# Performance work log

Measured on AMD Instinct MI355X. Metric: run time of the kernel, lower is better.

The kernel has to match this reference:

```python
import math
import jax, jax.numpy as jnp
import numpy as np

D = 512        # encoder_dim
LLM = 4096     # llm_dim
H = 8          # heads
L = 2          # depth
FF = 4 * D     # feedforward hidden
DH = D // H    # head dim
EPS = 1e-5


def setup_inputs() -> dict:
    key = jax.random.key(0)
    ks = jax.random.split(key, 16)
    s_d = 1.0 / math.sqrt(D)
    s_ff = 1.0 / math.sqrt(FF)
    inp = {
        "x": jax.random.normal(ks[0], (1, 8192, D), dtype=jnp.float32),
        # per-layer params, leading dim L
        "ln1_g": jnp.ones((L, D), jnp.float32),
        "ln1_b": jnp.zeros((L, D), jnp.float32),
        "Wq": jax.random.normal(ks[1], (L, D, D), jnp.float32) * s_d,
        "Wk": jax.random.normal(ks[2], (L, D, D), jnp.float32) * s_d,
        "Wv": jax.random.normal(ks[3], (L, D, D), jnp.float32) * s_d,
        "Wo": jax.random.normal(ks[4], (L, D, D), jnp.float32) * s_d,
        "bo": jnp.zeros((L, D), jnp.float32),
        "ln2_g": jnp.ones((L, D), jnp.float32),
        "ln2_b": jnp.zeros((L, D), jnp.float32),
        "W1": jax.random.normal(ks[5], (L, D, FF), jnp.float32) * s_d,
        "b1": jnp.zeros((L, FF), jnp.float32),
        "W2": jax.random.normal(ks[6], (L, FF, D), jnp.float32) * s_ff,
        "b2": jnp.zeros((L, D), jnp.float32),
        # final projector (xavier-like)
        "proj_W": jax.random.normal(ks[7], (D, LLM), jnp.float32) * math.sqrt(2.0 / (D + LLM)),
        "proj_b": jnp.zeros((LLM,), jnp.float32),
    }
    return inp


def _layernorm(h, g, b):
    mu = jnp.mean(h, axis=-1, keepdims=True)
    var = jnp.var(h, axis=-1, keepdims=True)
    return (h - mu) * jax.lax.rsqrt(var + EPS) * g + b


def _sinusoidal_pe(n, d):
    pos = jnp.arange(n, dtype=jnp.float32)[:, None]
    div = jnp.exp(jnp.arange(0, d, 2, dtype=jnp.float32) * (-math.log(10000.0) / d))
    pe = jnp.zeros((n, d), jnp.float32)
    pe = pe.at[:, 0::2].set(jnp.sin(pos * div))
    pe = pe.at[:, 1::2].set(jnp.cos(pos * div))
    return pe


def reference(x, ln1_g, ln1_b, Wq, Wk, Wv, Wo, bo, ln2_g, ln2_b, W1, b1, W2, b2, proj_W, proj_b):
    B, N, _ = x.shape
    x = x + _sinusoidal_pe(N, D)[None]  # positional encoding (dropout = identity at eval)
    scale = DH ** -0.5
    for l in range(L):
        # --- linear self-attention block (PreNorm + residual) ---
        h = _layernorm(x, ln1_g[l], ln1_b[l])
        q = (h @ Wq[l]).reshape(B, N, H, DH).transpose(0, 2, 1, 3)  # bhnd
        k = (h @ Wk[l]).reshape(B, N, H, DH).transpose(0, 2, 1, 3)
        v = (h @ Wv[l]).reshape(B, N, H, DH).transpose(0, 2, 1, 3)
        q = jax.nn.softmax(q, axis=-1) * scale        # softmax over feature dim
        k = jax.nn.softmax(k, axis=-2)                # softmax over sequence dim
        ctx = jnp.einsum('bhnd,bhne->bhde', k, v)     # small [B,H,DH,DH] context
        o = jnp.einsum('bhnd,bhde->bhne', q, ctx)
        o = o.transpose(0, 2, 1, 3).reshape(B, N, D)
        x = x + (o @ Wo[l] + bo[l])
        # --- feedforward block (PreNorm + residual, exact GELU) ---
        h = _layernorm(x, ln2_g[l], ln2_b[l])
        x = x + (jax.nn.gelu(h @ W1[l] + b1[l], approximate=False) @ W2[l] + b2[l])
    x = jnp.squeeze(x, 0)  # batch==1, matches torch x.squeeze(0)
    return x @ proj_W + proj_b  # [N, LLM]
```

## Files before the change

### kernel.cpp

```cpp
#include <hip/hip_runtime.h>
#include <hip/hip_bf16.h>
#include <math.h>

constexpr int N_SEQ = 8192;
constexpr int D     = 512;
constexpr int NH    = 8;
constexpr int FFDIM = 2048;
constexpr int LLMD  = 4096;
constexpr int NLAYER= 2;

typedef __bf16 bf16x8 __attribute__((ext_vector_type(8)));
typedef float  f32x4  __attribute__((ext_vector_type(4)));
typedef unsigned short u16x8 __attribute__((ext_vector_type(8)));

__device__ __forceinline__ unsigned short f2bf(float x) {
  unsigned u = __builtin_bit_cast(unsigned, x);
  unsigned r = (u + 0x7FFFu + ((u >> 16) & 1u)) >> 16;
  return (unsigned short)r;
}
__device__ __forceinline__ float bf2f(unsigned short u) {
  unsigned x = ((unsigned)u) << 16;
  return __builtin_bit_cast(float, x);
}

#define GLOAD16(g, l)                                                        \
  __builtin_amdgcn_global_load_lds(                                          \
      (const __attribute__((address_space(1))) void*)(g),                    \
      (__attribute__((address_space(3))) void*)(l), 16, 0, 0)

__global__ __launch_bounds__(256) void prep_kernel(const float* __restrict__ Wq,
                                                   const float* __restrict__ Wk,
                                                   const float* __restrict__ Wv,
                                                   const float* __restrict__ Wo,
                                                   const float* __restrict__ W1,
                                                   const float* __restrict__ W2,
                                                   const float* __restrict__ Wp,
                                                   unsigned short* __restrict__ WT,
                                                   const float* __restrict__ xin,
                                                   unsigned short* __restrict__ Xr,
                                                   unsigned short* __restrict__ Hb,
                                                   const float* __restrict__ g,
                                                   const float* __restrict__ b) {
  int bid = blockIdx.x;
  if (bid >= 8192) {
    int row  = ((bid - 8192) * 256 + (int)threadIdx.x) >> 6;
    int lane = threadIdx.x & 63;
    const float* p = xin + (size_t)row * D + lane * 8;
    float x[8];
#pragma unroll
    for (int i = 0; i < 8; ++i) {
      int d = lane * 8 + i;
      float freq = __expf((float)(d & ~1) * (-9.210340371976184f / 512.0f));
      float arg = (float)row * freq;
      float pe = (d & 1) ? cosf(arg) : sinf(arg);
      x[i] = p[i] + pe;
    }
    float s = 0.f, sq = 0.f;
#pragma unroll
    for (int i = 0; i < 8; ++i) { s += x[i]; sq += x[i] * x[i]; }
#pragma unroll
    for (int o = 32; o > 0; o >>= 1) { s += __shfl_xor(s, o); sq += __shfl_xor(sq, o); }
    float mu  = s * (1.0f / D);
    float var = sq * (1.0f / D) - mu * mu;
    float rs  = rsqrtf(var + 1e-5f);
    u16x8 xr, r;
#pragma unroll
    for (int i = 0; i < 8; ++i) {
      xr[i] = f2bf(x[i]);
      r[i]  = f2bf((x[i] - mu) * rs * g[lane * 8 + i] + b[lane * 8 + i]);
    }
    *(u16x8*)(Xr + (size_t)row * D + lane * 8) = xr;
    *(u16x8*)(Hb + (size_t)row * D + lane * 8) = r;
    return;
  }
  const float* src; unsigned short* dst; int K, N, tile;
  if (bid < 2048) {
    int mat = bid >> 8; int w = mat >> 1, l = mat & 1;
    const float* s4 = (w == 0) ? Wq : (w == 1) ? Wk : (w == 2) ? Wv : Wo;
    src = s4 + (size_t)l * 262144;
    dst = WT + ((size_t)l * 4 + w) * 262144;
    K = 512; N = 512; tile = bid & 255;
  } else if (bid < 4096) {
    int b2 = bid - 2048; int l = b2 >> 10;
    src = W1 + (size_t)l * 1048576; dst = WT + 2097152 + (size_t)l * 1048576;
    K = 512; N = 2048; tile = b2 & 1023;
  } else if (bid < 6144) {
    int b2 = bid - 4096; int l = b2 >> 10;
    src = W2 + (size_t)l * 1048576; dst = WT + 4194304 + (size_t)l * 1048576;
    K = 2048; N = 512; tile = b2 & 1023;
  } else {
    src = Wp; dst = WT + 6291456; K = 512; N = 4096; tile = bid - 6144;
  }
  int tilesN = N >> 5;
  int bk = (tile / tilesN) << 5, bn = (tile % tilesN) << 5;
  __shared__ float s[32][33];
  int r = threadIdx.x >> 5, c = threadIdx.x & 31;
#pragma unroll
  for (int i = 0; i < 4; ++i)
    s[r + 8 * i][c] = src[(size_t)(bk + r + 8 * i) * N + bn + c];
  __syncthreads();
#pragma unroll
  for (int i = 0; i < 4; ++i) {
    int rr = r + 8 * i;
    dst[(size_t)(bn + rr) * K + bk + c] = f2bf(s[c][rr]);
  }
}

__global__ __launch_bounds__(256) void ln_bf16(const unsigned short* __restrict__ in,
                                               unsigned short* __restrict__ out,
                                               const float* __restrict__ g,
                                               const float* __restrict__ b) {
  int row  = (blockIdx.x * 256 + threadIdx.x) >> 6;
  int lane = threadIdx.x & 63;
  u16x8 v = *(const u16x8*)(in + (size_t)row * D + lane * 8);
  float x[8];
#pragma unroll
  for (int i = 0; i < 8; ++i) x[i] = bf2f(v[i]);
  float s = 0.f, sq = 0.f;
#pragma unroll
  for (int i = 0; i < 8; ++i) { s += x[i]; sq += x[i] * x[i]; }
#pragma unroll
  for (int o = 32; o > 0; o >>= 1) { s += __shfl_xor(s, o); sq += __shfl_xor(sq, o); }
  float mu  = s * (1.0f / D);
  float var = sq * (1.0f / D) - mu * mu;
  float rs  = rsqrtf(var + 1e-5f);
  f32x4 g0 = *(const f32x4*)(g + lane * 8);
  f32x4 g1 = *(const f32x4*)(g + lane * 8 + 4);
  f32x4 b0 = *(const f32x4*)(b + lane * 8);
  f32x4 b1 = *(const f32x4*)(b + lane * 8 + 4);
  u16x8 r;
#pragma unroll
  for (int i = 0; i < 4; ++i) r[i]     = f2bf((x[i] - mu) * rs * g0[i] + b0[i]);
#pragma unroll
  for (int i = 0; i < 4; ++i) r[i + 4] = f2bf((x[i + 4] - mu) * rs * g1[i] + b1[i]);
  *(u16x8*)(out + (size_t)row * D + lane * 8) = r;
}

template <int FLAGS, int BN>
__global__ __launch_bounds__(256) void mgemm2(const unsigned short* __restrict__ A,
                                              const unsigned short* __restrict__ Bt,
                                              const float* __restrict__ bias,
                                              const unsigned short* __restrict__ resb,
                                              float* __restrict__ C,
                                              unsigned short* __restrict__ Cb,
                                              int M, int N, int K) {
  constexpr int WNI  = BN / 32;
  constexpr int NBUF = (BN == 128) ? 3 : 4;
  __shared__ unsigned short As[NBUF][128][32];
  __shared__ unsigned short Bs[NBUF][BN][32];
  const int tid = threadIdx.x;
  const int lane = tid & 63, wv = tid >> 6;
  const int nwg = gridDim.x * gridDim.y;
  int bid = blockIdx.y * gridDim.x + blockIdx.x;
  bid = (bid & 7) * (nwg >> 3) + (bid >> 3);
  const int bm = (bid / gridDim.x) * 128, bn = (bid % gridDim.x) * BN;
  const int wr = (wv >> 1) * 64, wc = (wv & 1) * (BN / 2);
  f32x4 acc[4][WNI] = {};

  const int srA = wv * 32 + (lane >> 2);
  const int sc  = (lane & 3) * 8;
  const unsigned short* Ap0 = A + (size_t)(bm + srA) * K + sc;
  const unsigned short* Ap1 = Ap0 + (size_t)16 * K;
  const int srB = wv * (BN / 4) + (lane >> 2);
  const unsigned short* Bp0 = Bt + (size_t)(bn + srB) * K + sc;
  const unsigned short* Bp1 = Bp0 + (size_t)16 * K;
  const int kh = (lane >> 4) * 8;
  const int fr = lane & 15;

  auto stage = [&](int bb, int k0) {
    GLOAD16(Ap0 + k0, &As[bb][srA][sc]);
    GLOAD16(Ap1 + k0, &As[bb][srA + 16][sc]);
    GLOAD16(Bp0 + k0, &Bs[bb][srB][sc]);
    if constexpr (BN == 128) GLOAD16(Bp1 + k0, &Bs[bb][srB + 16][sc]);
  };

  const int nt = K >> 5;
#pragma unroll
  for (int i = 0; i < NBUF - 1; ++i) stage(i, i << 5);
  int cur = 0;
  for (int t = 0; t < nt; ++t) {
    __builtin_amdgcn_sched_barrier(0);
    if constexpr (BN == 128)
      asm volatile("s_waitcnt vmcnt(4)" ::: "memory");
    else
      asm volatile("s_waitcnt vmcnt(6)" ::: "memory");
    __builtin_amdgcn_s_barrier();
    __builtin_amdgcn_sched_barrier(0);
    bf16x8 af[4], bfv[WNI];
#pragma unroll
    for (int mi = 0; mi < 4; ++mi)
      af[mi] = *(const bf16x8*)&As[cur][wr + mi * 16 + fr][kh];
#pragma unroll
    for (int ni = 0; ni < WNI; ++ni)
      bfv[ni] = *(const bf16x8*)&Bs[cur][wc + ni * 16 + fr][kh];
    if (t + NBUF - 1 < nt) {
      int tgt = cur - 1; if (tgt < 0) tgt += NBUF;
      stage(tgt, (t + NBUF - 1) << 5);
    }
#pragma unroll
    for (int mi = 0; mi < 4; ++mi)
#pragma unroll
      for (int ni = 0; ni < WNI; ++ni)
        acc[mi][ni] = __builtin_amdgcn_mfma_f32_16x16x32_bf16(af[mi], bfv[ni], acc[mi][ni], 0, 0, 0);
    ++cur; if (cur == NBUF) cur = 0;
  }

  const int r4 = (lane >> 4) * 4, cc = lane & 15;
#pragma unroll
  for (int mi = 0; mi < 4; ++mi) {
#pragma unroll
    for (int ni = 0; ni < WNI; ++ni) {
      int col = bn + wc + ni * 16 + cc;
      float bsv = (FLAGS & 1) ? bias[col] : 0.0f;
      f32x4 v = acc[mi][ni];
#pragma unroll
      for (int j = 0; j < 4; ++j) {
        int row = bm + wr + mi * 16 + r4 + j;
        float x = v[j] + bsv;
        if (FLAGS & 2) x = 0.5f * x * (1.0f + erff(x * 0.7071067811865475f));
        if (FLAGS & 4) x += bf2f(resb[(size_t)row * N + col]);
        if (!(FLAGS & 16)) C[(size_t)row * N + col] = x;
        if (FLAGS & 8) Cb[(size_t)row * N + col] = f2bf(x);
      }
    }
  }
}

__global__ __launch_bounds__(256) void qkv_gemm(const unsigned short* __restrict__ A,
                                                const unsigned short* __restrict__ Bt,
                                                unsigned short* __restrict__ Qb,
                                                unsigned short* __restrict__ Kb,
                                                unsigned short* __restrict__ Vb,
                                                float* __restrict__ pm,
                                                float* __restrict__ ps) {
  constexpr int K = 512;
  __shared__ unsigned short As[3][128][32];
  __shared__ unsigned short Bs[3][128][32];
  const int tid = threadIdx.x;
  const int lane = tid & 63, wv = tid >> 6;
  const int nwg = gridDim.x * gridDim.y;
  int bid = blockIdx.y * gridDim.x + blockIdx.x;
  bid = (bid & 7) * (nwg >> 3) + (bid >> 3);
  const int bm = (bid / gridDim.x) * 128, bn = (bid % gridDim.x) * 128;
  const int bmy = bid / gridDim.x;
  const int wr = (wv >> 1) * 64, wc = (wv & 1) * 64;
  f32x4 acc[4][4] = {};

  const int srA = wv * 32 + (lane >> 2);
  const int sc  = (lane & 3) * 8;
  const unsigned short* Ap0 = A + (size_t)(bm + srA) * K + sc;
  const unsigned short* Ap1 = Ap0 + (size_t)16 * K;
  const unsigned short* Bp0 = Bt + (size_t)(bn + srA) * K + sc;
  const unsigned short* Bp1 = Bp0 + (size_t)16 * K;
  const int kh = (lane >> 4) * 8;
  const int fr = lane & 15;

  auto stage = [&](int bb, int k0) {
    GLOAD16(Ap0 + k0, &As[bb][srA][sc]);
    GLOAD16(Ap1 + k0, &As[bb][srA + 16][sc]);
    GLOAD16(Bp0 + k0, &Bs[bb][srA][sc]);
    GLOAD16(Bp1 + k0, &Bs[bb][srA + 16][sc]);
  };

  stage(0, 0);
  stage(1, 32);
  int cur = 0;
  for (int t = 0; t < 16; ++t) {
    __builtin_amdgcn_sched_barrier(0);
    asm volatile("s_waitcnt vmcnt(4)" ::: "memory");
    __builtin_amdgcn_s_barrier();
    __builtin_amdgcn_sched_barrier(0);
    bf16x8 af[4], bfv[4];
#pragma unroll
    for (int mi = 0; mi < 4; ++mi)
      af[mi] = *(const bf16x8*)&As[cur][wr + mi * 16 + fr][kh];
#pragma unroll
    for (int ni = 0; ni < 4; ++ni)
      bfv[ni] = *(const bf16x8*)&Bs[cur][wc + ni * 16 + fr][kh];
    if (t + 2 < 16) {
      int tgt = cur - 1; if (tgt < 0) tgt += 3;
      stage(tgt, (t + 2) << 5);
    }
#pragma unroll
    for (int mi = 0; mi < 4; ++mi)
#pragma unroll
      for (int ni = 0; ni < 4; ++ni)
        acc[mi][ni] = __builtin_amdgcn_mfma_f32_16x16x32_bf16(af[mi], bfv[ni], acc[mi][ni], 0, 0, 0);
    ++cur; if (cur == 3) cur = 0;
  }

  const int r4 = (lane >> 4) * 4, cc = lane & 15;
  if (bn < 512) {
#pragma unroll
    for (int mi = 0; mi < 4; ++mi) {
#pragma unroll
      for (int j = 0; j < 4; ++j) {
        float v0 = acc[mi][0][j], v1 = acc[mi][1][j];
        float v2 = acc[mi][2][j], v3 = acc[mi][3][j];
        float m = fmaxf(fmaxf(v0, v1), fmaxf(v2, v3));
        m = fmaxf(m, __shfl_xor(m, 1)); m = fmaxf(m, __shfl_xor(m, 2));
        m = fmaxf(m, __shfl_xor(m, 4)); m = fmaxf(m, __shfl_xor(m, 8));
        float e0 = __expf(v0 - m), e1 = __expf(v1 - m);
        float e2 = __expf(v2 - m), e3 = __expf(v3 - m);
        float s = e0 + e1 + e2 + e3;
        s += __shfl_xor(s, 1); s += __shfl_xor(s, 2);
        s += __shfl_xor(s, 4); s += __shfl_xor(s, 8);
        float w = 0.125f / s;
        int row = bm + wr + mi * 16 + r4 + j;
        unsigned short* qr = Qb + (size_t)row * 512 + bn + wc + cc;
        qr[0] = f2bf(e0 * w); qr[16] = f2bf(e1 * w);
        qr[32] = f2bf(e2 * w); qr[48] = f2bf(e3 * w);
      }
    }
  } else if (bn < 1024) {
    int colb = bn - 512 + wc + cc;
    int prow = bmy * 2 + (wr ? 1 : 0);
#pragma unroll
    for (int ni = 0; ni < 4; ++ni) {
      float kf[4][4];
      float m = -1e30f;
#pragma unroll
      for (int mi = 0; mi < 4; ++mi)
#pragma unroll
        for (int j = 0; j < 4; ++j) {
          unsigned short kr = f2bf(acc[mi][ni][j]);
          Kb[(size_t)(bm + wr + mi * 16 + r4 + j) * 512 + colb + ni * 16] = kr;
          kf[mi][j] = bf2f(kr);
          m = fmaxf(m, kf[mi][j]);
        }
      m = fmaxf(m, __shfl_xor(m, 16));
      m = fmaxf(m, __shfl_xor(m, 32));
      float s = 0.f;
#pragma unroll
      for (int mi = 0; mi < 4; ++mi)
#pragma unroll
        for (int j = 0; j < 4; ++j) s += __expf(kf[mi][j] - m);
      s += __shfl_xor(s, 16);
      s += __shfl_xor(s, 32);
      if (lane < 16) {
        pm[(size_t)prow * 512 + colb + ni * 16] = m;
        ps[(size_t)prow * 512 + colb + ni * 16] = s;
      }
    }
  } else {
    int colv = bn - 1024 + wc + cc;
#pragma unroll
    for (int mi = 0; mi < 4; ++mi)
#pragma unroll
      for (int ni = 0; ni < 4; ++ni) {
        f32x4 v = acc[mi][ni];
#pragma unroll
        for (int j = 0; j < 4; ++j)
          Vb[(size_t)(bm + wr + mi * 16 + r4 + j) * 512 + colv + ni * 16] = f2bf(v[j]);
      }
  }
}

__global__ __launch_bounds__(256) void ctx_kernel(const unsigned short* __restrict__ kb,
                                                  const unsigned short* __restrict__ vb,
                                                  const float* __restrict__ pm,
                                                  const float* __restrict__ ps,
                                                  float* __restrict__ part) {
  int chunk = blockIdx.x, h = blockIdx.y, t = threadIdx.x;
  __shared__ unsigned short kst[64 * 256];
  __shared__ unsigned short vst[64 * 256];
  __shared__ float qm[4][64], qsum[4][64], scm[64], sci[64];
  {
    int c = t & 63, qt = t >> 6;
    float m = -1e30f, s = 0.f;
    for (int r = qt * 32; r < qt * 32 + 32; ++r) {
      float vm = pm[(size_t)r * 512 + h * 64 + c];
      float vp = ps[(size_t)r * 512 + h * 64 + c];
      float nm = fmaxf(m, vm);
      s = s * __expf(m - nm) + vp * __expf(vm - nm);
      m = nm;
    }
    qm[qt][c] = m; qsum[qt][c] = s;
  }
  __syncthreads();
  if (t < 64) {
    float M = fmaxf(fmaxf(qm[0][t], qm[1][t]), fmaxf(qm[2][t], qm[3][t]));
    float S = qsum[0][t] * __expf(qm[0][t] - M) + qsum[1][t] * __expf(qm[1][t] - M)
            + qsum[2][t] * __expf(qm[2][t] - M) + qsum[3][t] * __expf(qm[3][t] - M);
    scm[t] = M; sci[t] = 1.0f / S;
  }
  __syncthreads();
  size_t rowbase = (size_t)chunk * 256;
  for (int i = t; i < 4096; i += 256) {
    int n = i >> 4, c4 = (i & 15) * 4;
    ushort4 k4 = *(const ushort4*)&kb[(rowbase + n) * 512 + h * 64 + c4];
    ushort4 v4 = *(const ushort4*)&vb[(rowbase + n) * 512 + h * 64 + c4];
    unsigned short kr[4] = {
      f2bf(__expf(bf2f(k4.x) - scm[c4 + 0]) * sci[c4 + 0]),
      f2bf(__expf(bf2f(k4.y) - scm[c4 + 1]) * sci[c4 + 1]),
      f2bf(__expf(bf2f(k4.z) - scm[c4 + 2]) * sci[c4 + 2]),
      f2bf(__expf(bf2f(k4.w) - scm[c4 + 3]) * sci[c4 + 3])};
    unsigned short vr[4] = {v4.x, v4.y, v4.z, v4.w};
#pragma unroll
    for (int j = 0; j < 4; ++j) {
      int d = c4 + j;
      int byt = (d * 512 + n * 2) ^ ((d & 7) << 4);
      *(unsigned short*)((char*)kst + byt) = kr[j];
      *(unsigned short*)((char*)vst + byt) = vr[j];
    }
  }
  __syncthreads();
  int lane = t & 63, wv = t >> 6;
  int fr = lane & 15, kh = (lane >> 4) * 8;
  f32x4 acc[4] = {};
  int d = wv * 16 + fr;
#pragma unroll
  for (int kk = 0; kk < 8; ++kk) {
    int abyt = (d * 512 + (kk * 32 + kh) * 2) ^ ((d & 7) << 4);
    bf16x8 af = *(const bf16x8*)((const char*)kst + abyt);
#pragma unroll
    for (int ni = 0; ni < 4; ++ni) {
      int e = ni * 16 + fr;
      int bbyt = (e * 512 + (kk * 32 + kh) * 2) ^ ((e & 7) << 4);
      bf16x8 bv = *(const bf16x8*)((const char*)vst + bbyt);
      acc[ni] = __builtin_amdgcn_mfma_f32_16x16x32_bf16(af, bv, acc[ni], 0, 0, 0);
    }
  }
  int r4 = (lane >> 4) * 4, cc = lane & 15;
  float* pb = &part[((size_t)h * 32 + chunk) * 4096];
#pragma unroll
  for (int ni = 0; ni < 4; ++ni)
#pragma unroll
    for (int j = 0; j < 4; ++j)
      pb[(wv * 16 + r4 + j) * 64 + ni * 16 + cc] = acc[ni][j];
}

__global__ __launch_bounds__(256) void ctx_reduce_kernel(const float* __restrict__ part,
                                                         float* __restrict__ ctx) {
  int idx = blockIdx.x * 256 + threadIdx.x;
  int h = idx >> 12, de = idx & 4095;
  float s = 0.f;
#pragma unroll 8
  for (int c = 0; c < 32; ++c) s += part[((size_t)h * 32 + c) * 4096 + de];
  ctx[(size_t)h * 4096 + de] = s;
}

__global__ __launch_bounds__(256) void ctxw2_kernel(const float* __restrict__ ctx,
                                                    const float* __restrict__ Wo,
                                                    unsigned short* __restrict__ WPT) {
  int ct = blockIdx.x, h = blockIdx.y, t = threadIdx.x;
  __shared__ float cs[64][64];
  __shared__ float wo[64][64];
  for (int i = t; i < 4096; i += 256) {
    cs[i >> 6][i & 63] = ctx[(size_t)h * 4096 + i];
    wo[i >> 6][i & 63] = Wo[(size_t)(h * 64 + (i >> 6)) * 512 + ct * 64 + (i & 63)];
  }
  __syncthreads();
  int cl = t & 63, dg = (t >> 6) * 16;
  float accv[16];
#pragma unroll
  for (int j = 0; j < 16; ++j) accv[j] = 0.f;
  for (int e = 0; e < 64; ++e) {
    float w = wo[e][cl];
#pragma unroll
    for (int j = 0; j < 16; ++j) accv[j] = fmaf(cs[dg + j][e], w, accv[j]);
  }
  u16x8 o0, o1;
#pragma unroll
  for (int j = 0; j < 8; ++j) { o0[j] = f2bf(accv[j]); o1[j] = f2bf(accv[j + 8]); }
  unsigned short* dst = WPT + (size_t)(ct * 64 + cl) * 512 + h * 64 + dg;
  *(u16x8*)dst = o0;
  *(u16x8*)(dst + 8) = o1;
}

extern "C" void kernel_launch(void* const* d_in, const int* in_sizes, int n_in,
                              void* d_out, int out_size, void* d_ws, size_t ws_size,
                              hipStream_t stream) {
  const float* x_in  = (const float*)d_in[0];
  const float* ln1_g = (const float*)d_in[1];
  const float* ln1_b = (const float*)d_in[2];
  const float* Wq    = (const float*)d_in[3];
  const float* Wk    = (const float*)d_in[4];
  const float* Wv    = (const float*)d_in[5];
  const float* Wo    = (const float*)d_in[6];
  const float* bo    = (const float*)d_in[7];
  const float* ln2_g = (const float*)d_in[8];
  const float* ln2_b = (const float*)d_in[9];
  const float* W1    = (const float*)d_in[10];
  const float* b1    = (const float*)d_in[11];
  const float* W2    = (const float*)d_in[12];
  const float* b2    = (const float*)d_in[13];
  const float* projW = (const float*)d_in[14];
  const float* projb = (const float*)d_in[15];
  float* out = (float*)d_out;
  float* ws  = (float*)d_ws;
  constexpr size_t M1 = 1u << 20;

  float* CTXP = ws;
  float* PM   = ws + 1 * M1;
  float* PS   = PM + 65536;
  float* CTX  = PS + 65536;
  unsigned short* Xr  = (unsigned short*)(ws + 2 * M1);
  unsigned short* Qb  = (unsigned short*)(ws + 4 * M1);
  unsigned short* Kb  = (unsigned short*)(ws + 6 * M1);
  unsigned short* Vb  = (unsigned short*)(ws + 8 * M1);
  unsigned short* Hb  = (unsigned short*)(ws + 10 * M1);
  unsigned short* FFH = (unsigned short*)(ws + 12 * M1);
  unsigned short* WT  = (unsigned short*)(ws + 20 * M1);
  unsigned short* WPT = (unsigned short*)(ws + 24 * M1);

  prep_kernel<<<10240, 256, 0, stream>>>(Wq, Wk, Wv, Wo, W1, W2, projW, WT,
                                         x_in, Xr, Hb, ln1_g, ln1_b);

  dim3 gqkv(1536 / 128, N_SEQ / 128);
  dim3 g512n(512 / 64, N_SEQ / 128);
  dim3 gff1(FFDIM / 128, N_SEQ / 128);
  dim3 gproj(LLMD / 128, N_SEQ / 128);

  for (int l = 0; l < NLAYER; ++l) {
    const unsigned short* WQKV = WT + (size_t)l * 1048576;
    const unsigned short* W1T  = WT + 2097152 + (size_t)l * 1048576;
    const unsigned short* W2T  = WT + 4194304 + (size_t)l * 1048576;

    qkv_gemm<<<gqkv, 256, 0, stream>>>(Hb, WQKV, Qb, Kb, Vb, PM, PS);
    ctx_kernel<<<dim3(32, NH), 256, 0, stream>>>(Kb, Vb, PM, PS, CTXP);
    ctx_reduce_kernel<<<128, 256, 0, stream>>>(CTXP, CTX);
    ctxw2_kernel<<<dim3(8, NH), 256, 0, stream>>>(CTX, Wo + (size_t)l * D * D, WPT);
    mgemm2<29, 64><<<g512n, 256, 0, stream>>>(Qb, WPT, bo + l * D, Xr, nullptr,
                                              Xr, N_SEQ, 512, 512);
    ln_bf16<<<N_SEQ / 4, 256, 0, stream>>>(Xr, Hb, ln2_g + l * D, ln2_b + l * D);
    mgemm2<27, 128><<<gff1, 256, 0, stream>>>(Hb, W1T, b1 + l * FFDIM, nullptr,
                                              nullptr, FFH, N_SEQ, FFDIM, 512);
    mgemm2<29, 64><<<g512n, 256, 0, stream>>>(FFH, W2T, b2 + l * D, Xr, nullptr,
                                              Xr, N_SEQ, 512, 2048);
    if (l != NLAYER - 1)
      ln_bf16<<<N_SEQ / 4, 256, 0, stream>>>(Xr, Hb, ln1_g + (l + 1) * D,
                                             ln1_b + (l + 1) * D);
  }
  mgemm2<1, 128><<<gproj, 256, 0, stream>>>(Xr, WT + 6291456, projb, nullptr,
                                            out, nullptr, N_SEQ, LLMD, 512);
}
```

Baseline: 365.6 us.

## Fold LayerNorm into following GEMMs via row stats and gamma-scaled weights

Replaces the LayerNorm kernels that wrote a normalized bf16 activation buffer with a small row-statistics kernel that stores only mean and rstd per row. Gamma is folded into the transposed bf16 weights, and per-column sums of gamma*W and beta*W are precomputed, so the QKV and FF1 GEMMs read the raw residual and apply rs*(acc - mu*s1) + bw in the epilogue. This removes a full activation write and read per LayerNorm. The cost is an extra precompute kernel and some numerical risk, since the un-normalized residual is fed to the bf16 MMA and the mean is subtracted after accumulation (cancellation).

```diff
diff --git a/kernel.cpp b/kernel.cpp
--- a/kernel.cpp
+++ b/kernel.cpp
@@ -27,6 +27,8 @@
   __builtin_amdgcn_global_load_lds(                                          \
       (const __attribute__((address_space(1))) void*)(g),                    \
       (__attribute__((address_space(3))) void*)(l), 16, 0, 0)
+
+constexpr int SV_S1Q = 0, SV_BWQ = 3072, SV_S1F = 6144, SV_BWF = 10240;
 
 __global__ __launch_bounds__(256) void prep_kernel(const float* __restrict__ Wq,
                                                    const float* __restrict__ Wk,
@@ -38,9 +40,9 @@
                                                    unsigned short* __restrict__ WT,
                                                    const float* __restrict__ xin,
                                                    unsigned short* __restrict__ Xr,
-                                                   unsigned short* __restrict__ Hb,
-                                                   const float* __restrict__ g,
-                                                   const float* __restrict__ b) {
+                                                   float2* __restrict__ RST,
+                                                   const float* __restrict__ ln1g,
+                                                   const float* __restrict__ ln2g) {
   int bid = blockIdx.x;
   if (bid >= 8192) {
     int row  = ((bid - 8192) * 256 + (int)threadIdx.x) >> 6;
@@ -63,27 +65,27 @@
     float mu  = s * (1.0f / D);
     float var = sq * (1.0f / D) - mu * mu;
     float rs  = rsqrtf(var + 1e-5f);
-    u16x8 xr, r;
-#pragma unroll
-    for (int i = 0; i < 8; ++i) {
-      xr[i] = f2bf(x[i]);
-      r[i]  = f2bf((x[i] - mu) * rs * g[lane * 8 + i] + b[lane * 8 + i]);
-    }
+    u16x8 xr;
+#pragma unroll
+    for (int i = 0; i < 8; ++i) xr[i] = f2bf(x[i]);
     *(u16x8*)(Xr + (size_t)row * D + lane * 8) = xr;
-    *(u16x8*)(Hb + (size_t)row * D + lane * 8) = r;
+    if (lane == 0) RST[row] = make_float2(mu, rs);
     return;
   }
   const float* src; unsigned short* dst; int K, N, tile;
+  const float* gv = nullptr;
   if (bid < 2048) {
     int mat = bid >> 8; int w = mat >> 1, l = mat & 1;
     const float* s4 = (w == 0) ? Wq : (w == 1) ? Wk : (w == 2) ? Wv : Wo;
     src = s4 + (size_t)l * 262144;
     dst = WT + ((size_t)l * 4 + w) * 262144;
     K = 512; N = 512; tile = bid & 255;
+    if (w < 3) gv = ln1g + l * 512;
   } else if (bid < 4096) {
     int b2 = bid - 2048; int l = b2 >> 10;
     src = W1 + (size_t)l * 1048576; dst = WT + 2097152 + (size_t)l * 1048576;
     K = 512; N = 2048; tile = b2 & 1023;
+    gv = ln2g + l * 512;
   } else if (bid < 6144) {
     int b2 = bid - 4096; int l = b2 >> 10;
     src = W2 + (size_t)l * 1048576; dst = WT + 4194304 + (size_t)l * 1048576;
@@ -99,41 +101,64 @@
   for (int i = 0; i < 4; ++i)
     s[r + 8 * i][c] = src[(size_t)(bk + r + 8 * i) * N + bn + c];
   __syncthreads();
+  float gk = gv ? gv[bk + c] : 1.0f;
 #pragma unroll
   for (int i = 0; i < 4; ++i) {
     int rr = r + 8 * i;
-    dst[(size_t)(bn + rr) * K + bk + c] = f2bf(s[c][rr]);
-  }
-}
-
-__global__ __launch_bounds__(256) void ln_bf16(const unsigned short* __restrict__ in,
-                                               unsigned short* __restrict__ out,
-                                               const float* __restrict__ g,
-                                               const float* __restrict__ b) {
+    dst[(size_t)(bn + rr) * K + bk + c] = f2bf(s[c][rr] * gk);
+  }
+}
+
+__global__ __launch_bounds__(256) void vecprep_kernel(const float* __restrict__ Wq,
+                                                      const float* __restrict__ Wk,
+                                                      const float* __restrict__ Wv,
+                                                      const float* __restrict__ W1,
+                                                      const float* __restrict__ ln1g,
+                                                      const float* __restrict__ ln1b,
+                                                      const float* __restrict__ ln2g,
+                                                      const float* __restrict__ ln2b,
+                                                      float* __restrict__ SV) {
+  int bid = blockIdx.x, t = threadIdx.x;
+  const float* W; const float* g; const float* b;
+  int N, c0; float* s1o; float* bwo;
+  if (bid < 12) {
+    int l = bid / 6, m = (bid % 6) >> 1, chunk = bid & 1;
+    W = ((m == 0) ? Wq : (m == 1) ? Wk : Wv) + (size_t)l * 262144;
+    g = ln1g + l * 512; b = ln1b + l * 512;
+    N = 512; c0 = chunk * 256;
+    s1o = SV + SV_S1Q + l * 1536 + m * 512 + c0;
+    bwo = SV + SV_BWQ + l * 1536 + m * 512 + c0;
+  } else {
+    int b2 = bid - 12; int l = b2 >> 3, chunk = b2 & 7;
+    W = W1 + (size_t)l * 1048576;
+    g = ln2g + l * 512; b = ln2b + l * 512;
+    N = 2048; c0 = chunk * 256;
+    s1o = SV + SV_S1F + l * 2048 + c0;
+    bwo = SV + SV_BWF + l * 2048 + c0;
+  }
+  float s1 = 0.f, bw = 0.f;
+  for (int k = 0; k < 512; ++k) {
+    float w = W[(size_t)k * N + c0 + t];
+    s1 = fmaf(g[k], w, s1);
+    bw = fmaf(b[k], w, bw);
+  }
+  s1o[t] = s1;
+  bwo[t] = bw;
+}
+
+__global__ __launch_bounds__(256) void rowstats_kernel(const unsigned short* __restrict__ in,
+                                                       float2* __restrict__ RST) {
   int row  = (blockIdx.x * 256 + threadIdx.x) >> 6;
   int lane = threadIdx.x & 63;
   u16x8 v = *(const u16x8*)(in + (size_t)row * D + lane * 8);
-  float x[8];
-#pragma unroll
-  for (int i = 0; i < 8; ++i) x[i] = bf2f(v[i]);
   float s = 0.f, sq = 0.f;
 #pragma unroll
-  for (int i = 0; i < 8; ++i) { s += x[i]; sq += x[i] * x[i]; }
+  for (int i = 0; i < 8; ++i) { float x = bf2f(v[i]); s += x; sq += x * x; }
 #pragma unroll
   for (int o = 32; o > 0; o >>= 1) { s += __shfl_xor(s, o); sq += __shfl_xor(sq, o); }
   float mu  = s * (1.0f / D);
   float var = sq * (1.0f / D) - mu * mu;
-  float rs  = rsqrtf(var + 1e-5f);
-  f32x4 g0 = *(const f32x4*)(g + lane * 8);
-  f32x4 g1 = *(const f32x4*)(g + lane * 8 + 4);
-  f32x4 b0 = *(const f32x4*)(b + lane * 8);
-  f32x4 b1 = *(const f32x4*)(b + lane * 8 + 4);
-  u16x8 r;
-#pragma unroll
-  for (int i = 0; i < 4; ++i) r[i]     = f2bf((x[i] - mu) * rs * g0[i] + b0[i]);
-#pragma unroll
-  for (int i = 0; i < 4; ++i) r[i + 4] = f2bf((x[i + 4] - mu) * rs * g1[i] + b1[i]);
-  *(u16x8*)(out + (size_t)row * D + lane * 8) = r;
+  if (lane == 0) RST[row] = make_float2(mu, rsqrtf(var + 1e-5f));
 }
 
 template <int FLAGS, int BN>
@@ -143,6 +168,9 @@
                                               const unsigned short* __restrict__ resb,
                                               float* __restrict__ C,
                                               unsigned short* __restrict__ Cb,
+                                              const float2* __restrict__ rst,
+                                              const float* __restrict__ s1v,
+                                              const float* __restrict__ bwv,
                                               int M, int N, int K) {
   constexpr int WNI  = BN / 32;
   constexpr int NBUF = (BN == 128) ? 3 : 4;
@@ -206,6 +234,22 @@
   }
 
   const int r4 = (lane >> 4) * 4, cc = lane & 15;
+  float muv[4][4], rsv[4][4];
+  float s1c[WNI], bwc[WNI];
+  if (FLAGS & 32) {
+#pragma unroll
+    for (int mi = 0; mi < 4; ++mi)
+#pragma unroll
+      for (int j = 0; j < 4; ++j) {
+        float2 f2 = rst[bm + wr + mi * 16 + r4 + j];
+        muv[mi][j] = f2.x; rsv[mi][j] = f2.y;
+      }
+#pragma unroll
+    for (int ni = 0; ni < WNI; ++ni) {
+      int col = bn + wc + ni * 16 + cc;
+      s1c[ni] = s1v[col]; bwc[ni] = bwv[col];
+    }
+  }
 #pragma unroll
   for (int mi = 0; mi < 4; ++mi) {
 #pragma unroll
@@ -216,7 +260,10 @@
 #pragma unroll
       for (int j = 0; j < 4; ++j) {
         int row = bm + wr + mi * 16 + r4 + j;
-        float x = v[j] + bsv;
+        float x = v[j];
+        if (FLAGS & 32)
+          x = rsv[mi][j] * (x - muv[mi][j] * s1c[ni]) + bwc[ni];
+        x += bsv;
         if (FLAGS & 2) x = 0.5f * x * (1.0f + erff(x * 0.7071067811865475f));
         if (FLAGS & 4) x += bf2f(resb[(size_t)row * N + col]);
         if (!(FLAGS & 16)) C[(size_t)row * N + col] = x;
@@ -232,7 +279,10 @@
                                                 unsigned short* __restrict__ Kb,
                                                 unsigned short* __restrict__ Vb,
                                                 float* __restrict__ pm,
-                                                float* __restrict__ ps) {
+                                                float* __restrict__ ps,
+                                                const float2* __restrict__ rst,
+                                                const float* __restrict__ s1v,
+                                                const float* __restrict__ bwv) {
   constexpr int K = 512;
   __shared__ unsigned short As[3][128][32];
   __shared__ unsigned short Bs[3][128][32];
@@ -290,6 +340,29 @@
   }
 
   const int r4 = (lane >> 4) * 4, cc = lane & 15;
+  {
+    float muv[4][4], rsv[4][4], s1c[4], bwc[4];
+#pragma unroll
+    for (int mi = 0; mi < 4; ++mi)
+#pragma unroll
+      for (int j = 0; j < 4; ++j) {
+        float2 f2 = rst[bm + wr + mi * 16 + r4 + j];
+        muv[mi][j] = f2.x; rsv[mi][j] = f2.y;
+      }
+#pragma unroll
+    for (int ni = 0; ni < 4; ++ni) {
+      int n1536 = bn + wc + ni * 16 + cc;
+      s1c[ni] = s1v[n1536]; bwc[ni] = bwv[n1536];
+    }
+#pragma unroll
+    for (int mi = 0; mi < 4; ++mi)
+#pragma unroll
+      for (int ni = 0; ni < 4; ++ni)
+#pragma unroll
+        for (int j = 0; j < 4; ++j)
+          acc[mi][ni][j] = rsv[mi][j] * (acc[mi][ni][j] - muv[mi][j] * s1c[ni]) + bwc[ni];
+  }
+
   if (bn < 512) {
 #pragma unroll
     for (int mi = 0; mi < 4; ++mi) {
@@ -491,21 +564,24 @@
   float* ws  = (float*)d_ws;
   constexpr size_t M1 = 1u << 20;
 
-  float* CTXP = ws;
-  float* PM   = ws + 1 * M1;
-  float* PS   = PM + 65536;
-  float* CTX  = PS + 65536;
+  float*  CTXP = ws;
+  float*  PM   = ws + 1 * M1;
+  float*  PS   = PM + 65536;
+  float*  CTX  = PS + 65536;
+  float*  SV   = CTX + 32768;
+  float2* RST  = (float2*)(SV + 16384);
   unsigned short* Xr  = (unsigned short*)(ws + 2 * M1);
   unsigned short* Qb  = (unsigned short*)(ws + 4 * M1);
   unsigned short* Kb  = (unsigned short*)(ws + 6 * M1);
   unsigned short* Vb  = (unsigned short*)(ws + 8 * M1);
-  unsigned short* Hb  = (unsigned short*)(ws + 10 * M1);
-  unsigned short* FFH = (unsigned short*)(ws + 12 * M1);
-  unsigned short* WT  = (unsigned short*)(ws + 20 * M1);
-  unsigned short* WPT = (unsigned short*)(ws + 24 * M1);
+  unsigned short* FFH = (unsigned short*)(ws + 10 * M1);
+  unsigned short* WT  = (unsigned short*)(ws + 18 * M1);
+  unsigned short* WPT = (unsigned short*)(ws + 22 * M1);
 
   prep_kernel<<<10240, 256, 0, stream>>>(Wq, Wk, Wv, Wo, W1, W2, projW, WT,
-                                         x_in, Xr, Hb, ln1_g, ln1_b);
+                                         x_in, Xr, RST, ln1_g, ln2_g);
+  vecprep_kernel<<<28, 256, 0, stream>>>(Wq, Wk, Wv, W1, ln1_g, ln1_b,
+                                         ln2_g, ln2_b, SV);
 
   dim3 gqkv(1536 / 128, N_SEQ / 128);
   dim3 g512n(512 / 64, N_SEQ / 128);
@@ -517,21 +593,28 @@
     const unsigned short* W1T  = WT + 2097152 + (size_t)l * 1048576;
     const unsigned short* W2T  = WT + 4194304 + (size_t)l * 1048576;
 
-    qkv_gemm<<<gqkv, 256, 0, stream>>>(Hb, WQKV, Qb, Kb, Vb, PM, PS);
+    qkv_gemm<<<gqkv, 256, 0, stream>>>(Xr, WQKV, Qb, Kb, Vb, PM, PS,
+                                       RST, SV + SV_S1Q + l * 1536,
+                                       SV + SV_BWQ + l * 1536);
     ctx_kernel<<<dim3(32, NH), 256, 0, stream>>>(Kb, Vb, PM, PS, CTXP);
     ctx_reduce_kernel<<<128, 256, 0, stream>>>(CTXP, CTX);
     ctxw2_kernel<<<dim3(8, NH), 256, 0, stream>>>(CTX, Wo + (size_t)l * D * D, WPT);
     mgemm2<29, 64><<<g512n, 256, 0, stream>>>(Qb, WPT, bo + l * D, Xr, nullptr,
-                                              Xr, N_SEQ, 512, 512);
-    ln_bf16<<<N_SEQ / 4, 256, 0, stream>>>(Xr, Hb, ln2_g + l * D, ln2_b + l * D);
-    mgemm2<27, 128><<<gff1, 256, 0, stream>>>(Hb, W1T, b1 + l * FFDIM, nullptr,
-                                              nullptr, FFH, N_SEQ, FFDIM, 512);
+                                              Xr, nullptr, nullptr, nullptr,
+                                              N_SEQ, 512, 512);
+    rowstats_kernel<<<N_SEQ / 4, 256, 0, stream>>>(Xr, RST);
+    mgemm2<59, 128><<<gff1, 256, 0, stream>>>(Xr, W1T, b1 + l * FFDIM, nullptr,
+                                              nullptr, FFH, RST,
+                                              SV + SV_S1F + l * 2048,
+                                              SV + SV_BWF + l * 2048,
+                                              N_SEQ, FFDIM, 512);
     mgemm2<29, 64><<<g512n, 256, 0, stream>>>(FFH, W2T, b2 + l * D, Xr, nullptr,
-                                              Xr, N_SEQ, 512, 2048);
+                                              Xr, nullptr, nullptr, nullptr,
+                                              N_SEQ, 512, 2048);
     if (l != NLAYER - 1)
-      ln_bf16<<<N_SEQ / 4, 256, 0, stream>>>(Xr, Hb, ln1_g + (l + 1) * D,
-                                             ln1_b + (l + 1) * D);
+      rowstats_kernel<<<N_SEQ / 4, 256, 0, stream>>>(Xr, RST);
   }
   mgemm2<1, 128><<<gproj, 256, 0, stream>>>(Xr, WT + 6291456, projb, nullptr,
-                                            out, nullptr, N_SEQ, LLMD, 512);
-}
+                                            out, nullptr, nullptr, nullptr,
+                                            nullptr, N_SEQ, LLMD, 512);
+}
```

Result: slower. 416.3 us (+13.9%).
